# Performance work log

Measured on AMD Instinct MI355X. Metric: run time of the kernel, lower is better.

Reference implementation:

```python
import jax, jax.numpy as jnp
import numpy as np
import math

HIDDEN = 8
HEADS = 2
HEAD_DIM = HIDDEN // HEADS  # 4
MAX_SEQ = 102
B, S = 4096, 102


def _rotary_cache(seq_len, head_dim):
    # Matches _create_rotary_embeddings: dim = head_dim//2, inv_freq over arange(0, dim, 2)
    pos = jnp.arange(seq_len, dtype=jnp.float32)
    dim = head_dim // 2
    inv_freq = 1.0 / (10000.0 ** (jnp.arange(0, dim, 2, dtype=jnp.float32) / dim))
    sinusoid = pos[:, None] * inv_freq[None, :]           # [seq, dim//2] -> [102, 1]
    return jnp.stack([jnp.sin(sinusoid), jnp.cos(sinusoid)], axis=0)  # [2, seq, 1]


def _apply_rotary(x, cos, sin):
    # x: [B, H, S, hd]; cos/sin: [2, S, 1] (faithful to the source's buggy unpack,
    # which broadcasts the stacked sin/cos pair across the H==2 head dim)
    x2 = jnp.stack([-x[..., 1::2], x[..., ::2]], axis=-1).reshape(x.shape)
    return x * cos + x2 * sin


def setup_inputs() -> dict:
    key = jax.random.key(0)
    kq, kk, kv, k1, k2, k3, k4 = jax.random.split(key, 7)
    scale = 1.0 / math.sqrt(HIDDEN)
    return {
        "query": jax.random.normal(kq, (B, S, HIDDEN), dtype=jnp.float32),
        "key": jax.random.normal(kk, (B, S, HIDDEN), dtype=jnp.float32),
        "value": jax.random.normal(kv, (B, S, HIDDEN), dtype=jnp.float32),
        "wq": jax.random.normal(k1, (HIDDEN, HIDDEN), dtype=jnp.float32) * scale,
        "wk": jax.random.normal(k2, (HIDDEN, HIDDEN), dtype=jnp.float32) * scale,
        "wv": jax.random.normal(k3, (HIDDEN, HIDDEN), dtype=jnp.float32) * scale,
        "wo": jax.random.normal(k4, (HIDDEN, HIDDEN), dtype=jnp.float32) * scale,
    }


def reference(query, key, value, wq, wk, wv, wo):
    b, sq, _ = query.shape
    sk = key.shape[1]
    # nn.Linear (no bias): y = x @ W^T
    q = query @ wq.T
    k = key @ wk.T
    v = value @ wv.T
    # b n (h d) -> b h n d
    def split_heads(t, s):
        return t.reshape(b, s, HEADS, HEAD_DIM).transpose(0, 2, 1, 3)
    q = split_heads(q, sq)
    k = split_heads(k, sk)
    v = split_heads(v, sk)
    cache = _rotary_cache(MAX_SEQ, HEAD_DIM)
    sin_t = cache[:, :sq]  # [2, sq, 1] (named 'sin' in source, holds stacked sin/cos)
    cos_t = cache[:, :sk]  # [2, sk, 1]
    q = _apply_rotary(q, cos_t, sin_t)
    k = _apply_rotary(k, cos_t, sin_t)
    scale = 1.0 / math.sqrt(HEAD_DIM)
    # chunk_size = min(sk, 1024) = sk -> single chunk == full softmax attention
    scores = jnp.einsum('bhqd,bhkd->bhqk', q, k) * scale  # [B, H, Sq, Sk]
    attn = jax.nn.softmax(scores, axis=-1)
    out = jnp.einsum('bhqk,bhkd->bhqd', attn, v)
    # b h n d -> b n (h d)
    out = out.transpose(0, 2, 1, 3).reshape(b, sq, HIDDEN)
    return out @ wo.T
```

## Files before the change

### kernel.cpp

```cpp
#include <hip/hip_runtime.h>

#define NB 4096
#define SS 102
#define SSP 104
#define HID 8
#define NH 2
#define HD 4

typedef float v2f __attribute__((ext_vector_type(2)));

__global__ __launch_bounds__(256, 4) void mha_fused_kernel(
    const float* __restrict__ query, const float* __restrict__ key,
    const float* __restrict__ value, const float* __restrict__ wq,
    const float* __restrict__ wk, const float* __restrict__ wv,
    const float* __restrict__ wo, float* __restrict__ out)
{
    __shared__ float sRaw[3 * SS * HID];
    __shared__ float sQ[NH * SSP * HD];
    __shared__ float sK[NH * SS * HD];
    __shared__ float sV[NH * SS * HD];
    __shared__ float sW[4 * 64];

    const int t = threadIdx.x;
    const int b = blockIdx.x;

    if (t < 64)        sW[t] = wq[t];
    else if (t < 128)  sW[t] = wk[t - 64];
    else if (t < 192)  sW[t] = wv[t - 128];
    else               sW[t] = wo[t - 192];

    if (t >= 208 && t < 224) {
        const int z = t - 208;
        const int h = z >> 3, r = SS + ((z >> 2) & 1), d = z & 3;
        sQ[h * SSP * HD + r * HD + d] = 0.f;
    }

    {
        const float4* q4 = (const float4*)(query + (size_t)b * (SS * HID));
        const float4* k4 = (const float4*)(key   + (size_t)b * (SS * HID));
        const float4* v4 = (const float4*)(value + (size_t)b * (SS * HID));
        float4* sRaw4 = (float4*)sRaw;
        if (t < 204) {
            sRaw4[t]       = q4[t];
            sRaw4[204 + t] = k4[t];
            sRaw4[408 + t] = v4[t];
        }
    }
    __syncthreads();

    for (int p = t; p < 816; p += 256) {
        const int tensor = p / 408;
        const int pp = p % 408;
        const int s  = pp >> 2;
        const int pr = pp & 3;
        const int i0 = pr * 2, i1 = i0 + 1;
        const float* raw = sRaw + tensor * (SS * HID) + s * HID;
        const float* w   = sW + tensor * 64;
        float x0 = 0.f, x1 = 0.f;
#pragma unroll
        for (int j = 0; j < 8; ++j) {
            x0 += raw[j] * w[i0 * 8 + j];
            x1 += raw[j] * w[i1 * 8 + j];
        }
        const int h = i0 >> 2;
        float wr = (h == 0) ? sinf((float)s) : cosf((float)s);
        if (tensor == 0) wr *= 0.72134752044448170368f;
        const float r0 = (x0 - x1) * wr;
        const float r1 = (x1 + x0) * wr;
        const int d0 = i0 & 3;
        float* dst = (tensor == 0)
            ? (sQ + h * SSP * HD + s * HD + d0)
            : (sK + h * SS * HD + s * HD + d0);
        dst[0] = r0;
        dst[1] = r1;
    }
    for (int e = t; e < 816; e += 256) {
        const int s = e >> 3, i = e & 7;
        const float* raw = sRaw + 2 * (SS * HID) + s * HID;
        const float* w   = sW + 2 * 64 + i * 8;
        float x = 0.f;
#pragma unroll
        for (int j = 0; j < 8; ++j) x += raw[j] * w[j];
        const int h = i >> 2, d = i & 3;
        sV[h * SS * HD + s * HD + d] = x;
    }
    __syncthreads();

    const int h  = (t >= 32) ? 1 : 0;
    const int tb = t - h * 32;
    const bool active = (t < 58) && (tb < 26);
    v2f acc01[4] = {}, acc23[4] = {};
    v2f l01 = {0.f, 0.f}, l23 = {0.f, 0.f};
    if (active) {
        const float* qb = sQ + h * SSP * HD + (4 * tb) * HD;
        const float4 qa = ((const float4*)qb)[0];
        const float4 qB = ((const float4*)qb)[1];
        const float4 qc = ((const float4*)qb)[2];
        const float4 qd = ((const float4*)qb)[3];
        v2f q01[4] = {{qa.x, qB.x}, {qa.y, qB.y}, {qa.z, qB.z}, {qa.w, qB.w}};
        v2f q23[4] = {{qc.x, qd.x}, {qc.y, qd.y}, {qc.z, qd.z}, {qc.w, qd.w}};
        const float4* K4 = (const float4*)(sK + h * SS * HD);
        const float4* V4 = (const float4*)(sV + h * SS * HD);
        for (int k = 0; k < SS; ++k) {
            const float4 kk = K4[k];
            const float4 vv = V4[k];
            v2f s01 = q01[0] * kk.x + q01[1] * kk.y + q01[2] * kk.z + q01[3] * kk.w;
            v2f s23 = q23[0] * kk.x + q23[1] * kk.y + q23[2] * kk.z + q23[3] * kk.w;
            v2f p01, p23;
            p01.x = __builtin_amdgcn_exp2f(s01.x);
            p01.y = __builtin_amdgcn_exp2f(s01.y);
            p23.x = __builtin_amdgcn_exp2f(s23.x);
            p23.y = __builtin_amdgcn_exp2f(s23.y);
            l01 += p01; l23 += p23;
            acc01[0] += p01 * vv.x; acc01[1] += p01 * vv.y;
            acc01[2] += p01 * vv.z; acc01[3] += p01 * vv.w;
            acc23[0] += p23 * vv.x; acc23[1] += p23 * vv.y;
            acc23[2] += p23 * vv.z; acc23[3] += p23 * vv.w;
        }
    }
    __syncthreads();
    if (active) {
        const float l[4] = {l01.x, l01.y, l23.x, l23.y};
#pragma unroll
        for (int j = 0; j < 4; ++j) {
            const int row = 4 * tb + j;
            if (row < SS) {
                const float inv = 1.f / l[j];
                float* comb = sRaw + row * HID + h * HD;
                const v2f* accp = (j < 2) ? acc01 : acc23;
                const int c = j & 1;
                comb[0] = accp[0][c] * inv;
                comb[1] = accp[1][c] * inv;
                comb[2] = accp[2][c] * inv;
                comb[3] = accp[3][c] * inv;
            }
        }
    }
    __syncthreads();

    for (int e = t; e < 816; e += 256) {
        const int s = e >> 3, i = e & 7;
        const float* comb = sRaw + s * HID;
        const float* w    = sW + 3 * 64 + i * 8;
        float x = 0.f;
#pragma unroll
        for (int j = 0; j < 8; ++j) x += comb[j] * w[j];
        out[(size_t)b * (SS * HID) + e] = x;
    }
}

extern "C" void kernel_launch(void* const* d_in, const int* in_sizes, int n_in,
                              void* d_out, int out_size, void* d_ws, size_t ws_size,
                              hipStream_t stream) {
    const float* query = (const float*)d_in[0];
    const float* key   = (const float*)d_in[1];
    const float* value = (const float*)d_in[2];
    const float* wq    = (const float*)d_in[3];
    const float* wk    = (const float*)d_in[4];
    const float* wv    = (const float*)d_in[5];
    const float* wo    = (const float*)d_in[6];
    float* out = (float*)d_out;
    mha_fused_kernel<<<NB, 256, 0, stream>>>(query, key, value, wq, wk, wv, wo, out);
}
```

Baseline: 129.6 us.

## Split attention keys across four waves and precompute rotary table in shared memory

Attention is spread over all four waves: each wave takes one head and one half of the keys, each lane handles two query rows, and the two halves are combined through shared-memory partial sums. Previously only part of one wave did the whole attention loop. The change also precomputes sin/cos once per block into a shared table, issues global loads into registers before writing them to shared memory, and vectorises the small projections with float4 shared loads. The price is an extra partial-sum exchange and dropping the occupancy hint from launch bounds.

```diff
diff --git a/kernel.cpp b/kernel.cpp
--- a/kernel.cpp
+++ b/kernel.cpp
@@ -9,7 +9,7 @@
 
 typedef float v2f __attribute__((ext_vector_type(2)));
 
-__global__ __launch_bounds__(256, 4) void mha_fused_kernel(
+__global__ __launch_bounds__(256) void mha_fused_kernel(
     const float* __restrict__ query, const float* __restrict__ key,
     const float* __restrict__ value, const float* __restrict__ wq,
     const float* __restrict__ wk, const float* __restrict__ wv,
@@ -20,50 +20,58 @@
     __shared__ float sK[NH * SS * HD];
     __shared__ float sV[NH * SS * HD];
     __shared__ float sW[4 * 64];
+    __shared__ float sRot[2 * SS];
 
     const int t = threadIdx.x;
     const int b = blockIdx.x;
 
-    if (t < 64)        sW[t] = wq[t];
-    else if (t < 128)  sW[t] = wk[t - 64];
-    else if (t < 192)  sW[t] = wv[t - 128];
-    else               sW[t] = wo[t - 192];
+    float4 rq, rk, rv;
+    if (t < 204) {
+        const float4* q4 = (const float4*)(query + (size_t)b * (SS * HID));
+        const float4* k4 = (const float4*)(key   + (size_t)b * (SS * HID));
+        const float4* v4 = (const float4*)(value + (size_t)b * (SS * HID));
+        rq = q4[t]; rk = k4[t]; rv = v4[t];
+    }
+    float wreg;
+    {
+        const float* wsrc = (t < 64) ? wq : (t < 128) ? wk : (t < 192) ? wv : wo;
+        wreg = wsrc[t & 63];
+    }
 
-    if (t >= 208 && t < 224) {
-        const int z = t - 208;
+    if (t < SS)                    sRot[t] = sinf((float)t);
+    else if (t >= 128 && t < 230)  sRot[SS + (t - 128)] = cosf((float)(t - 128));
+
+    if (t >= 230 && t < 246) {
+        const int z = t - 230;
         const int h = z >> 3, r = SS + ((z >> 2) & 1), d = z & 3;
         sQ[h * SSP * HD + r * HD + d] = 0.f;
     }
 
-    {
-        const float4* q4 = (const float4*)(query + (size_t)b * (SS * HID));
-        const float4* k4 = (const float4*)(key   + (size_t)b * (SS * HID));
-        const float4* v4 = (const float4*)(value + (size_t)b * (SS * HID));
+    sW[t] = wreg;
+    if (t < 204) {
         float4* sRaw4 = (float4*)sRaw;
-        if (t < 204) {
-            sRaw4[t]       = q4[t];
-            sRaw4[204 + t] = k4[t];
-            sRaw4[408 + t] = v4[t];
-        }
+        sRaw4[t]       = rq;
+        sRaw4[204 + t] = rk;
+        sRaw4[408 + t] = rv;
     }
     __syncthreads();
 
     for (int p = t; p < 816; p += 256) {
-        const int tensor = p / 408;
-        const int pp = p % 408;
+        const int tensor = (p >= 408) ? 1 : 0;
+        const int pp = tensor ? (p - 408) : p;
         const int s  = pp >> 2;
         const int pr = pp & 3;
         const int i0 = pr * 2, i1 = i0 + 1;
-        const float* raw = sRaw + tensor * (SS * HID) + s * HID;
-        const float* w   = sW + tensor * 64;
-        float x0 = 0.f, x1 = 0.f;
-#pragma unroll
-        for (int j = 0; j < 8; ++j) {
-            x0 += raw[j] * w[i0 * 8 + j];
-            x1 += raw[j] * w[i1 * 8 + j];
-        }
-        const int h = i0 >> 2;
-        float wr = (h == 0) ? sinf((float)s) : cosf((float)s);
+        const float4* raw4 = (const float4*)(sRaw + tensor * (SS * HID) + s * HID);
+        const float4 ra = raw4[0], rb = raw4[1];
+        const float4* w0 = (const float4*)(sW + tensor * 64 + i0 * 8);
+        const float4 wa = w0[0], wb = w0[1], wc = w0[2], wd = w0[3];
+        float x0 = ra.x * wa.x + ra.y * wa.y + ra.z * wa.z + ra.w * wa.w
+                 + rb.x * wb.x + rb.y * wb.y + rb.z * wb.z + rb.w * wb.w;
+        float x1 = ra.x * wc.x + ra.y * wc.y + ra.z * wc.z + ra.w * wc.w
+                 + rb.x * wd.x + rb.y * wd.y + rb.z * wd.z + rb.w * wd.w;
+        const int h = pr >> 1;
+        float wr = sRot[h * SS + s];
         if (tensor == 0) wr *= 0.72134752044448170368f;
         const float r0 = (x0 - x1) * wr;
         const float r1 = (x1 + x0) * wr;
@@ -76,63 +84,80 @@
     }
     for (int e = t; e < 816; e += 256) {
         const int s = e >> 3, i = e & 7;
-        const float* raw = sRaw + 2 * (SS * HID) + s * HID;
-        const float* w   = sW + 2 * 64 + i * 8;
-        float x = 0.f;
-#pragma unroll
-        for (int j = 0; j < 8; ++j) x += raw[j] * w[j];
+        const float4* raw4 = (const float4*)(sRaw + 2 * (SS * HID) + s * HID);
+        const float4 ra = raw4[0], rb = raw4[1];
+        const float4* w0 = (const float4*)(sW + 2 * 64 + i * 8);
+        const float4 wa = w0[0], wb = w0[1];
+        const float x = ra.x * wa.x + ra.y * wa.y + ra.z * wa.z + ra.w * wa.w
+                      + rb.x * wb.x + rb.y * wb.y + rb.z * wb.z + rb.w * wb.w;
         const int h = i >> 2, d = i & 3;
         sV[h * SS * HD + s * HD + d] = x;
     }
     __syncthreads();
 
-    const int h  = (t >= 32) ? 1 : 0;
-    const int tb = t - h * 32;
-    const bool active = (t < 58) && (tb < 26);
-    v2f acc01[4] = {}, acc23[4] = {};
-    v2f l01 = {0.f, 0.f}, l23 = {0.f, 0.f};
-    if (active) {
-        const float* qb = sQ + h * SSP * HD + (4 * tb) * HD;
+    const int wv_  = t >> 6, lane = t & 63;
+    const int h    = wv_ >> 1;
+    const int kh   = wv_ & 1;
+    const bool act = lane < 52;
+    v2f acc0 = {0.f, 0.f}, acc1 = {0.f, 0.f}, acc2 = {0.f, 0.f}, acc3 = {0.f, 0.f};
+    v2f l = {0.f, 0.f};
+    if (act) {
+        const float* qb = sQ + h * SSP * HD + (2 * lane) * HD;
         const float4 qa = ((const float4*)qb)[0];
-        const float4 qB = ((const float4*)qb)[1];
-        const float4 qc = ((const float4*)qb)[2];
-        const float4 qd = ((const float4*)qb)[3];
-        v2f q01[4] = {{qa.x, qB.x}, {qa.y, qB.y}, {qa.z, qB.z}, {qa.w, qB.w}};
-        v2f q23[4] = {{qc.x, qd.x}, {qc.y, qd.y}, {qc.z, qd.z}, {qc.w, qd.w}};
-        const float4* K4 = (const float4*)(sK + h * SS * HD);
-        const float4* V4 = (const float4*)(sV + h * SS * HD);
-        for (int k = 0; k < SS; ++k) {
-            const float4 kk = K4[k];
-            const float4 vv = V4[k];
-            v2f s01 = q01[0] * kk.x + q01[1] * kk.y + q01[2] * kk.z + q01[3] * kk.w;
-            v2f s23 = q23[0] * kk.x + q23[1] * kk.y + q23[2] * kk.z + q23[3] * kk.w;
-            v2f p01, p23;
-            p01.x = __builtin_amdgcn_exp2f(s01.x);
-            p01.y = __builtin_amdgcn_exp2f(s01.y);
-            p23.x = __builtin_amdgcn_exp2f(s23.x);
-            p23.y = __builtin_amdgcn_exp2f(s23.y);
-            l01 += p01; l23 += p23;
-            acc01[0] += p01 * vv.x; acc01[1] += p01 * vv.y;
-            acc01[2] += p01 * vv.z; acc01[3] += p01 * vv.w;
-            acc23[0] += p23 * vv.x; acc23[1] += p23 * vv.y;
-            acc23[2] += p23 * vv.z; acc23[3] += p23 * vv.w;
+        const float4 qc = ((const float4*)qb)[1];
+        const v2f q0 = {qa.x, qc.x}, q1 = {qa.y, qc.y},
+                  q2 = {qa.z, qc.z}, q3 = {qa.w, qc.w};
+        const float4* K4 = (const float4*)(sK + h * SS * HD) + kh * 51;
+        const float4* V4 = (const float4*)(sV + h * SS * HD) + kh * 51;
+        float4 kk = K4[0], vvv = V4[0];
+#pragma unroll 2
+        for (int k = 1; k < 51; ++k) {
+            const float4 nk = K4[k], nv = V4[k];
+            v2f s = q0 * kk.x + q1 * kk.y + q2 * kk.z + q3 * kk.w;
+            v2f p;
+            p.x = __builtin_amdgcn_exp2f(s.x);
+            p.y = __builtin_amdgcn_exp2f(s.y);
+            l += p;
+            acc0 += p * vvv.x; acc1 += p * vvv.y;
+            acc2 += p * vvv.z; acc3 += p * vvv.w;
+            kk = nk; vvv = nv;
+        }
+        {
+            v2f s = q0 * kk.x + q1 * kk.y + q2 * kk.z + q3 * kk.w;
+            v2f p;
+            p.x = __builtin_amdgcn_exp2f(s.x);
+            p.y = __builtin_amdgcn_exp2f(s.y);
+            l += p;
+            acc0 += p * vvv.x; acc1 += p * vvv.y;
+            acc2 += p * vvv.z; acc3 += p * vvv.w;
         }
     }
+    if (act && kh == 1) {
+        float* part = sRaw + 816 + (h * SSP + 2 * lane) * 5;
+        part[0] = acc0.x; part[1] = acc1.x; part[2] = acc2.x;
+        part[3] = acc3.x; part[4] = l.x;
+        part[5] = acc0.y; part[6] = acc1.y; part[7] = acc2.y;
+        part[8] = acc3.y; part[9] = l.y;
+    }
     __syncthreads();
-    if (active) {
-        const float l[4] = {l01.x, l01.y, l23.x, l23.y};
+    if (act && kh == 0) {
+        const float* part = sRaw + 816 + (h * SSP + 2 * lane) * 5;
+        const float a0[2] = {acc0.x, acc0.y}, a1[2] = {acc1.x, acc1.y};
+        const float a2[2] = {acc2.x, acc2.y}, a3[2] = {acc3.x, acc3.y};
+        const float ll[2] = {l.x, l.y};
 #pragma unroll
-        for (int j = 0; j < 4; ++j) {
-            const int row = 4 * tb + j;
+        for (int j = 0; j < 2; ++j) {
+            const int row = 2 * lane + j;
             if (row < SS) {
-                const float inv = 1.f / l[j];
+                const float s0 = a0[j] + part[5 * j + 0];
+                const float s1 = a1[j] + part[5 * j + 1];
+                const float s2 = a2[j] + part[5 * j + 2];
+                const float s3 = a3[j] + part[5 * j + 3];
+                const float L  = ll[j] + part[5 * j + 4];
+                const float inv = 1.f / L;
                 float* comb = sRaw + row * HID + h * HD;
-                const v2f* accp = (j < 2) ? acc01 : acc23;
-                const int c = j & 1;
-                comb[0] = accp[0][c] * inv;
-                comb[1] = accp[1][c] * inv;
-                comb[2] = accp[2][c] * inv;
-                comb[3] = accp[3][c] * inv;
+                comb[0] = s0 * inv; comb[1] = s1 * inv;
+                comb[2] = s2 * inv; comb[3] = s3 * inv;
             }
         }
     }
@@ -140,11 +165,12 @@
 
     for (int e = t; e < 816; e += 256) {
         const int s = e >> 3, i = e & 7;
-        const float* comb = sRaw + s * HID;
-        const float* w    = sW + 3 * 64 + i * 8;
-        float x = 0.f;
-#pragma unroll
-        for (int j = 0; j < 8; ++j) x += comb[j] * w[j];
+        const float4* c4 = (const float4*)(sRaw + s * HID);
+        const float4 ca = c4[0], cb = c4[1];
+        const float4* w0 = (const float4*)(sW + 3 * 64 + i * 8);
+        const float4 wa = w0[0], wb = w0[1];
+        const float x = ca.x * wa.x + ca.y * wa.y + ca.z * wa.z + ca.w * wa.w
+                      + cb.x * wb.x + cb.y * wb.y + cb.z * wb.z + cb.w * wb.w;
         out[(size_t)b * (SS * HID) + e] = x;
     }
 }
```

Measured after the change: 118.6 us. 1.09x faster.
